# Kernel tuning notes

Hardware: AMD Instinct MI355X
Metric: run time of the kernel (lower is better)

The kernel has to match this reference:

```python
import jax, jax.numpy as jnp
import numpy as np

N_HEAD = 16
N_KV_HEAD = 4
HEAD_DIM = 64  # n_embd // n_head = 1024 // 16
N_EMBD = 1024


def _alibi_bias(T, n_head, head_dim):
    # slopes: start = 2**(-2**(-(log2(H)-3))); slope_i = start**(i+1)
    start = 2.0 ** (-2.0 ** (-(np.log2(n_head) - 3.0)))
    slopes = jnp.asarray(start ** np.arange(1, n_head + 1), dtype=jnp.float32)  # [H]
    rel = (jnp.arange(T, dtype=jnp.float32)[None, :]
           - jnp.arange(T, dtype=jnp.float32)[:, None])  # [T,T], rel[i,j] = j - i
    bias = slopes[:, None, None] * rel[None, :, :]  # [H,T,T]
    # Faithful to the torch module: masked_fill(-inf) is then OVERWRITTEN by
    # torch.tril, which zeroes the upper triangle. Net effect: lower-tri alibi
    # values, 0 above the diagonal (NO causal masking).
    bias = jnp.tril(bias)
    return bias * (head_dim ** -0.5)  # extra scale applied in forward


def setup_inputs() -> dict:
    key = jax.random.key(0)
    ks = jax.random.split(key, 5)
    B, T, C = 4, 2048, N_EMBD
    w_scale = 0.02
    return {
        "x": jax.random.normal(ks[0], (B, T, C), dtype=jnp.float32),
        "Wq": jax.random.normal(ks[1], (C, C), dtype=jnp.float32) * w_scale,
        "Wkv": jax.random.normal(ks[2], (2 * N_KV_HEAD * HEAD_DIM, C), dtype=jnp.float32) * w_scale,
        "Wproj": jax.random.normal(ks[3], (C, C), dtype=jnp.float32) * w_scale,
        "bproj": jnp.zeros((C,), dtype=jnp.float32),
    }


def reference(x, Wq, Wkv, Wproj, bproj):
    B, T, C = x.shape
    H, KVH, D = N_HEAD, N_KV_HEAD, HEAD_DIM
    ratio = H // KVH

    q = jnp.einsum('btc,ec->bte', x, Wq).reshape(B, T, H, D).transpose(0, 2, 1, 3)  # [B,H,T,D]
    kv = jnp.einsum('btc,ec->bte', x, Wkv)  # [B,T,2*KVH*D]
    k, v = jnp.split(kv, 2, axis=-1)
    k = k.reshape(B, T, KVH, D).transpose(0, 2, 1, 3)  # [B,KVH,T,D]
    v = v.reshape(B, T, KVH, D).transpose(0, 2, 1, 3)
    # torch .repeat tiles whole blocks: query head h uses kv head h % KVH
    k = jnp.tile(k, (1, ratio, 1, 1))  # [B,H,T,D]
    v = jnp.tile(v, (1, ratio, 1, 1))

    bias = _alibi_bias(T, H, D)  # [H,T,T], already *= D**-0.5
    scores = jnp.einsum('bhtd,bhsd->bhts', q, k) * (D ** -0.5) + bias[None]
    attn = jax.nn.softmax(scores, axis=-1)
    out = jnp.einsum('bhts,bhsd->bhtd', attn, v)  # [B,H,T,D]
    out = out.transpose(0, 2, 1, 3).reshape(B, T, C)
    return jnp.einsum('btc,ec->bte', out, Wproj) + bproj
```

## Files before the change

### kernel.cpp

```cpp
#include <hip/hip_runtime.h>
#include <hip/hip_bf16.h>
#include <cstdint>

typedef __bf16 bf16;
typedef bf16 bf16x4 __attribute__((ext_vector_type(4)));
typedef bf16 bf16x8 __attribute__((ext_vector_type(8)));
typedef float f32x4 __attribute__((ext_vector_type(4)));

#define MFMA16(a, b, c) __builtin_amdgcn_mfma_f32_16x16x32_bf16((a), (b), (c), 0, 0, 0)

__global__ void cast_f32_to_bf16(const float* __restrict__ src,
                                 bf16* __restrict__ dst, int n4) {
  int i = blockIdx.x * blockDim.x + threadIdx.x;
  if (i < n4) {
    const float4 v = ((const float4*)src)[i];
    bf16x4 o;
    o.x = (bf16)v.x; o.y = (bf16)v.y; o.z = (bf16)v.z; o.w = (bf16)v.w;
    ((bf16x4*)dst)[i] = o;
  }
}

__global__ __launch_bounds__(256, 2)
void gemm_qkv(const bf16* __restrict__ A, const bf16* __restrict__ B,
              bf16* __restrict__ qb, bf16* __restrict__ kb, bf16* __restrict__ vb) {
  constexpr int K = 1024;
  __shared__ bf16 sA[128 * 72];
  __shared__ bf16 sB[128 * 72];
  const int tid = threadIdx.x;
  const int lane = tid & 63, wid = tid >> 6;
  const int col = lane & 15, quad = lane >> 4;
  const int wm = wid >> 1, wn = wid & 1;
  const int m0 = blockIdx.y * 128, n0 = blockIdx.x * 128;

  f32x4 acc[4][4];
  const f32x4 z = {0.f, 0.f, 0.f, 0.f};
#pragma unroll
  for (int mi = 0; mi < 4; mi++)
#pragma unroll
    for (int ni = 0; ni < 4; ni++) acc[mi][ni] = z;

  for (int k0 = 0; k0 < K; k0 += 64) {
    __syncthreads();
#pragma unroll
    for (int c = 0; c < 4; ++c) {
      int idx = c * 256 + tid;
      int row = idx >> 3, kc = idx & 7;
      *(bf16x8*)&sA[row * 72 + kc * 8] =
          *(const bf16x8*)&A[(size_t)(m0 + row) * K + k0 + kc * 8];
      *(bf16x8*)&sB[row * 72 + kc * 8] =
          *(const bf16x8*)&B[(size_t)(n0 + row) * K + k0 + kc * 8];
    }
    __syncthreads();
#pragma unroll
    for (int ks = 0; ks < 2; ++ks) {
      const int kk = ks * 32 + quad * 8;
      bf16x8 af[4], bfr[4];
#pragma unroll
      for (int i = 0; i < 4; i++)
        af[i] = *(const bf16x8*)&sA[(wm * 64 + i * 16 + col) * 72 + kk];
#pragma unroll
      for (int i = 0; i < 4; i++)
        bfr[i] = *(const bf16x8*)&sB[(wn * 64 + i * 16 + col) * 72 + kk];
#pragma unroll
      for (int mi = 0; mi < 4; mi++)
#pragma unroll
        for (int ni = 0; ni < 4; ni++)
          acc[mi][ni] = MFMA16(af[mi], bfr[ni], acc[mi][ni]);
    }
  }
#pragma unroll
  for (int mi = 0; mi < 4; mi++) {
#pragma unroll
    for (int ni = 0; ni < 4; ni++) {
      const int e = n0 + wn * 64 + ni * 16 + col;
#pragma unroll
      for (int r = 0; r < 4; r++) {
        const int m = m0 + wm * 64 + mi * 16 + quad * 4 + r;
        const int bb = m >> 11, t = m & 2047;
        const bf16 val = (bf16)acc[mi][ni][r];
        if (e < 1024) {
          qb[(((size_t)bb * 16 + (e >> 6)) * 2048 + t) * 64 + (e & 63)] = val;
        } else if (e < 1280) {
          const int f = e - 1024;
          kb[(((size_t)bb * 4 + (f >> 6)) * 2048 + t) * 64 + (f & 63)] = val;
        } else {
          const int f = e - 1280;
          vb[(((size_t)bb * 4 + (f >> 6)) * 2048 + t) * 64 + (f & 63)] = val;
        }
      }
    }
  }
}

__global__ __launch_bounds__(256, 2)
void gemm_proj(const bf16* __restrict__ A, const bf16* __restrict__ B,
               const float* __restrict__ bias, float* __restrict__ out) {
  constexpr int K = 1024;
  __shared__ bf16 sA[128 * 72];
  __shared__ bf16 sB[128 * 72];
  const int tid = threadIdx.x;
  const int lane = tid & 63, wid = tid >> 6;
  const int col = lane & 15, quad = lane >> 4;
  const int wm = wid >> 1, wn = wid & 1;
  const int m0 = blockIdx.y * 128, n0 = blockIdx.x * 128;

  f32x4 acc[4][4];
  const f32x4 z = {0.f, 0.f, 0.f, 0.f};
#pragma unroll
  for (int mi = 0; mi < 4; mi++)
#pragma unroll
    for (int ni = 0; ni < 4; ni++) acc[mi][ni] = z;

  for (int k0 = 0; k0 < K; k0 += 64) {
    __syncthreads();
#pragma unroll
    for (int c = 0; c < 4; ++c) {
      int idx = c * 256 + tid;
      int row = idx >> 3, kc = idx & 7;
      *(bf16x8*)&sA[row * 72 + kc * 8] =
          *(const bf16x8*)&A[(size_t)(m0 + row) * K + k0 + kc * 8];
      *(bf16x8*)&sB[row * 72 + kc * 8] =
          *(const bf16x8*)&B[(size_t)(n0 + row) * K + k0 + kc * 8];
    }
    __syncthreads();
#pragma unroll
    for (int ks = 0; ks < 2; ++ks) {
      const int kk = ks * 32 + quad * 8;
      bf16x8 af[4], bfr[4];
#pragma unroll
      for (int i = 0; i < 4; i++)
        af[i] = *(const bf16x8*)&sA[(wm * 64 + i * 16 + col) * 72 + kk];
#pragma unroll
      for (int i = 0; i < 4; i++)
        bfr[i] = *(const bf16x8*)&sB[(wn * 64 + i * 16 + col) * 72 + kk];
#pragma unroll
      for (int mi = 0; mi < 4; mi++)
#pragma unroll
        for (int ni = 0; ni < 4; ni++)
          acc[mi][ni] = MFMA16(af[mi], bfr[ni], acc[mi][ni]);
    }
  }
#pragma unroll
  for (int mi = 0; mi < 4; mi++) {
#pragma unroll
    for (int ni = 0; ni < 4; ni++) {
      const int e = n0 + wn * 64 + ni * 16 + col;
      const float be = bias[e];
#pragma unroll
      for (int r = 0; r < 4; r++) {
        const int m = m0 + wm * 64 + mi * 16 + quad * 4 + r;
        out[(size_t)m * 1024 + e] = acc[mi][ni][r] + be;
      }
    }
  }
}

__global__ __launch_bounds__(256, 2)
void attn_alibi(const bf16* __restrict__ qb, const bf16* __restrict__ kb,
                const bf16* __restrict__ vb, bf16* __restrict__ ob) {
  __shared__ bf16 sK[64 * 72];
  __shared__ bf16 sVt[64 * 72];
  __shared__ bf16 sPt[4][64 * 72];
  __shared__ float sL[4][64];
  const int tid = threadIdx.x;
  const int lane = tid & 63, wid = tid >> 6;
  const int col = lane & 15, quad = lane >> 4;
  const int bh = blockIdx.y;
  const int b = bh >> 4, h = bh & 15, kvh = h & 3;
  const int qbase = __builtin_amdgcn_readfirstlane(blockIdx.x * 256 + wid * 64);

  const bf16* qptr = qb + ((size_t)(b * 16 + h) * 2048 + qbase) * 64;
  const bf16* kptr = kb + ((size_t)(b * 4 + kvh) * 2048) * 64;
  const bf16* vptr = vb + ((size_t)(b * 4 + kvh) * 2048) * 64;

  bf16x8 bq[4][2];
#pragma unroll
  for (int ni = 0; ni < 4; ni++)
#pragma unroll
    for (int ks = 0; ks < 2; ks++)
      bq[ni][ks] = *(const bf16x8*)&qptr[(ni * 16 + col) * 64 + ks * 32 + quad * 8];

  f32x4 O[4][4];
  const f32x4 z = {0.f, 0.f, 0.f, 0.f};
#pragma unroll
  for (int mi = 0; mi < 4; mi++)
#pragma unroll
    for (int nd = 0; nd < 4; nd++) O[mi][nd] = z;
  float lsum[4] = {0.f, 0.f, 0.f, 0.f};

  const float c1 = 0.125f * 1.44269504f;
  const float cb = exp2f(-0.5f * (float)(h + 1)) * c1;
  const int qoff = quad * 4 - col;

  for (int c0 = 0; c0 < 2048; c0 += 64) {
    __syncthreads();
#pragma unroll
    for (int c = 0; c < 2; c++) {
      int idx = c * 256 + tid, row = idx >> 3, kc = idx & 7;
      *(bf16x8*)&sK[row * 72 + kc * 8] =
          *(const bf16x8*)&kptr[(size_t)(c0 + row) * 64 + kc * 8];
    }
#pragma unroll
    for (int c = 0; c < 2; c++) {
      int idx = c * 256 + tid, row = idx >> 3, dc = idx & 7;
      bf16x8 v = *(const bf16x8*)&vptr[(size_t)(c0 + row) * 64 + dc * 8];
      const int blk = row >> 3, rl = row & 7;
#pragma unroll
      for (int j = 0; j < 8; j++)
        sVt[(dc * 8 + j) * 72 + ((blk ^ dc) << 3) + rl] = v[j];
    }
    __syncthreads();

    f32x4 S[4][4];
#pragma unroll
    for (int mi = 0; mi < 4; mi++)
#pragma unroll
      for (int ni = 0; ni < 4; ni++) S[mi][ni] = z;
#pragma unroll
    for (int ks = 0; ks < 2; ks++) {
      bf16x8 ak[4];
#pragma unroll
      for (int mi = 0; mi < 4; mi++)
        ak[mi] = *(const bf16x8*)&sK[(mi * 16 + col) * 72 + ks * 32 + quad * 8];
#pragma unroll
      for (int mi = 0; mi < 4; mi++)
#pragma unroll
        for (int ni = 0; ni < 4; ni++)
          S[mi][ni] = MFMA16(ak[mi], bq[ni][ks], S[mi][ni]);
    }

    bf16* sp = sPt[wid];
#pragma unroll
    for (int ni = 0; ni < 4; ni++) {
      f32x4 p[4];
#pragma unroll
      for (int mi = 0; mi < 4; mi++) {
        const int U = c0 + mi * 16 - qbase - ni * 16;
        if (U <= -15) {
          const float bb = cb * (float)(U + qoff);
#pragma unroll
          for (int r = 0; r < 4; r++)
            p[mi][r] = __builtin_amdgcn_exp2f(S[mi][ni][r] * c1 + (bb + cb * (float)r));
        } else if (U >= 16) {
#pragma unroll
          for (int r = 0; r < 4; r++)
            p[mi][r] = __builtin_amdgcn_exp2f(S[mi][ni][r] * c1);
        } else {
          const float relf = (float)(U + qoff);
#pragma unroll
          for (int r = 0; r < 4; r++) {
            const float rr = relf + (float)r;
            const float bb = (rr <= 0.f) ? cb * rr : 0.f;
            p[mi][r] = __builtin_amdgcn_exp2f(S[mi][ni][r] * c1 + bb);
          }
        }
      }
      f32x4 t = (p[0] + p[1]) + (p[2] + p[3]);
      lsum[ni] += (t.x + t.y) + (t.z + t.w);
#pragma unroll
      for (int mi = 0; mi < 4; mi++) {
        bf16x4 w;
#pragma unroll
        for (int r = 0; r < 4; r++) w[r] = (bf16)p[mi][r];
        *(bf16x4*)&sp[(ni * 16 + col) * 72 + mi * 16 + quad * 4] = w;
      }
    }

#pragma unroll
    for (int ks = 0; ks < 2; ks++) {
      bf16x8 ap[4], bv[4];
#pragma unroll
      for (int mi = 0; mi < 4; mi++)
        ap[mi] = *(const bf16x8*)&sp[(mi * 16 + col) * 72 + ks * 32 + quad * 8];
#pragma unroll
      for (int nd = 0; nd < 4; nd++) {
        const int d = nd * 16 + col;
        bv[nd] = *(const bf16x8*)&sVt[d * 72 + (((ks * 4 + quad) ^ (d >> 3)) << 3)];
      }
#pragma unroll
      for (int mi = 0; mi < 4; mi++)
#pragma unroll
        for (int nd = 0; nd < 4; nd++)
          O[mi][nd] = MFMA16(ap[mi], bv[nd], O[mi][nd]);
    }
  }

#pragma unroll
  for (int ni = 0; ni < 4; ni++) {
    float l = lsum[ni];
    l += __shfl_xor(l, 16);
    l += __shfl_xor(l, 32);
    lsum[ni] = l;
  }
  __syncthreads();
  if (quad == 0) {
#pragma unroll
    for (int ni = 0; ni < 4; ni++) sL[wid][ni * 16 + col] = lsum[ni];
  }
  __syncthreads();

#pragma unroll
  for (int mi = 0; mi < 4; mi++) {
    const f32x4 lv = *(const f32x4*)&sL[wid][mi * 16 + quad * 4];
#pragma unroll
    for (int r = 0; r < 4; r++) {
      const float inv = 1.0f / lv[r];
      const int t = qbase + mi * 16 + quad * 4 + r;
#pragma unroll
      for (int nd = 0; nd < 4; nd++) {
        ob[((size_t)b * 2048 + t) * 1024 + h * 64 + nd * 16 + col] =
            (bf16)(O[mi][nd][r] * inv);
      }
    }
  }
}

extern "C" void kernel_launch(void* const* d_in, const int* in_sizes, int n_in,
                              void* d_out, int out_size, void* d_ws, size_t ws_size,
                              hipStream_t stream) {
  const float* x     = (const float*)d_in[0];
  const float* Wq    = (const float*)d_in[1];
  const float* Wkv   = (const float*)d_in[2];
  const float* Wproj = (const float*)d_in[3];
  const float* bproj = (const float*)d_in[4];
  float* out = (float*)d_out;

  bf16* xb  = (bf16*)d_ws;
  bf16* w1b = xb  + 8388608;
  bf16* wpb = w1b + 1572864;
  bf16* qb  = wpb + 1048576;
  bf16* kb  = qb  + 8388608;
  bf16* vb  = kb  + 2097152;
  bf16* aob = vb  + 2097152;

  cast_f32_to_bf16<<<8192, 256, 0, stream>>>(x, xb, 2097152);
  cast_f32_to_bf16<<<1024, 256, 0, stream>>>(Wq, w1b, 262144);
  cast_f32_to_bf16<<<512, 256, 0, stream>>>(Wkv, w1b + 1048576, 131072);
  cast_f32_to_bf16<<<1024, 256, 0, stream>>>(Wproj, wpb, 262144);

  gemm_qkv<<<dim3(12, 64), 256, 0, stream>>>(xb, w1b, qb, kb, vb);
  attn_alibi<<<dim3(8, 64), 256, 0, stream>>>(qb, kb, vb, aob);
  gemm_proj<<<dim3(8, 64), 256, 0, stream>>>(aob, wpb, bproj, out);
}
```

Measured before the change: 276.9 us.

## Use async global-to-LDS loads with XOR swizzle in GEMMs and prefetch K/V in attention

Both GEMM kernels now load their A and B tiles with global_load_lds direct-to-LDS transfers into an unpadded, XOR-swizzled layout, and the fragment reads apply the matching swizzle. This drops the register round trip and the padding while aiming to avoid LDS bank conflicts. The attention kernel prefetches the next K/V chunk into registers while the current one is in use, overlapping global latency with compute. It uses lgkmcnt-only barriers, and the async LDS loads rely on __syncthreads to wait for vmcnt, which is a correctness risk.

```diff
diff --git a/kernel.cpp b/kernel.cpp
--- a/kernel.cpp
+++ b/kernel.cpp
@@ -8,6 +8,16 @@
 typedef float f32x4 __attribute__((ext_vector_type(4)));
 
 #define MFMA16(a, b, c) __builtin_amdgcn_mfma_f32_16x16x32_bf16((a), (b), (c), 0, 0, 0)
+
+__device__ inline void async16(const bf16* g, bf16* l) {
+  __builtin_amdgcn_global_load_lds(
+      (const __attribute__((address_space(1))) void*)g,
+      (__attribute__((address_space(3))) void*)l, 16, 0, 0);
+}
+
+__device__ inline void lds_barrier() {
+  asm volatile("s_waitcnt lgkmcnt(0)\n\ts_barrier" ::: "memory");
+}
 
 __global__ void cast_f32_to_bf16(const float* __restrict__ src,
                                  bf16* __restrict__ dst, int n4) {
@@ -24,13 +34,14 @@
 void gemm_qkv(const bf16* __restrict__ A, const bf16* __restrict__ B,
               bf16* __restrict__ qb, bf16* __restrict__ kb, bf16* __restrict__ vb) {
   constexpr int K = 1024;
-  __shared__ bf16 sA[128 * 72];
-  __shared__ bf16 sB[128 * 72];
+  __shared__ bf16 sA[128 * 64];
+  __shared__ bf16 sB[128 * 64];
   const int tid = threadIdx.x;
   const int lane = tid & 63, wid = tid >> 6;
   const int col = lane & 15, quad = lane >> 4;
   const int wm = wid >> 1, wn = wid & 1;
   const int m0 = blockIdx.y * 128, n0 = blockIdx.x * 128;
+  const int c7 = col & 7;
 
   f32x4 acc[4][4];
   const f32x4 z = {0.f, 0.f, 0.f, 0.f};
@@ -43,24 +54,24 @@
     __syncthreads();
 #pragma unroll
     for (int c = 0; c < 4; ++c) {
-      int idx = c * 256 + tid;
-      int row = idx >> 3, kc = idx & 7;
-      *(bf16x8*)&sA[row * 72 + kc * 8] =
-          *(const bf16x8*)&A[(size_t)(m0 + row) * K + k0 + kc * 8];
-      *(bf16x8*)&sB[row * 72 + kc * 8] =
-          *(const bf16x8*)&B[(size_t)(n0 + row) * K + k0 + kc * 8];
+      const int idx = c * 256 + tid;
+      const int row = idx >> 3, kc = idx & 7;
+      const int gkc = kc ^ (row & 7);
+      async16(&A[(size_t)(m0 + row) * K + k0 + gkc * 8], &sA[idx * 8]);
+      async16(&B[(size_t)(n0 + row) * K + k0 + gkc * 8], &sB[idx * 8]);
     }
     __syncthreads();
 #pragma unroll
     for (int ks = 0; ks < 2; ++ks) {
-      const int kk = ks * 32 + quad * 8;
       bf16x8 af[4], bfr[4];
 #pragma unroll
       for (int i = 0; i < 4; i++)
-        af[i] = *(const bf16x8*)&sA[(wm * 64 + i * 16 + col) * 72 + kk];
+        af[i] = *(const bf16x8*)&sA[(wm * 64 + i * 16 + col) * 64 +
+                                    (((ks * 4 + quad) ^ c7) << 3)];
 #pragma unroll
       for (int i = 0; i < 4; i++)
-        bfr[i] = *(const bf16x8*)&sB[(wn * 64 + i * 16 + col) * 72 + kk];
+        bfr[i] = *(const bf16x8*)&sB[(wn * 64 + i * 16 + col) * 64 +
+                                     (((ks * 4 + quad) ^ c7) << 3)];
 #pragma unroll
       for (int mi = 0; mi < 4; mi++)
 #pragma unroll
@@ -96,13 +107,14 @@
 void gemm_proj(const bf16* __restrict__ A, const bf16* __restrict__ B,
                const float* __restrict__ bias, float* __restrict__ out) {
   constexpr int K = 1024;
-  __shared__ bf16 sA[128 * 72];
-  __shared__ bf16 sB[128 * 72];
+  __shared__ bf16 sA[128 * 64];
+  __shared__ bf16 sB[128 * 64];
   const int tid = threadIdx.x;
   const int lane = tid & 63, wid = tid >> 6;
   const int col = lane & 15, quad = lane >> 4;
   const int wm = wid >> 1, wn = wid & 1;
   const int m0 = blockIdx.y * 128, n0 = blockIdx.x * 128;
+  const int c7 = col & 7;
 
   f32x4 acc[4][4];
   const f32x4 z = {0.f, 0.f, 0.f, 0.f};
@@ -115,24 +127,24 @@
     __syncthreads();
 #pragma unroll
     for (int c = 0; c < 4; ++c) {
-      int idx = c * 256 + tid;
-      int row = idx >> 3, kc = idx & 7;
-      *(bf16x8*)&sA[row * 72 + kc * 8] =
-          *(const bf16x8*)&A[(size_t)(m0 + row) * K + k0 + kc * 8];
-      *(bf16x8*)&sB[row * 72 + kc * 8] =
-          *(const bf16x8*)&B[(size_t)(n0 + row) * K + k0 + kc * 8];
+      const int idx = c * 256 + tid;
+      const int row = idx >> 3, kc = idx & 7;
+      const int gkc = kc ^ (row & 7);
+      async16(&A[(size_t)(m0 + row) * K + k0 + gkc * 8], &sA[idx * 8]);
+      async16(&B[(size_t)(n0 + row) * K + k0 + gkc * 8], &sB[idx * 8]);
     }
     __syncthreads();
 #pragma unroll
     for (int ks = 0; ks < 2; ++ks) {
-      const int kk = ks * 32 + quad * 8;
       bf16x8 af[4], bfr[4];
 #pragma unroll
       for (int i = 0; i < 4; i++)
-        af[i] = *(const bf16x8*)&sA[(wm * 64 + i * 16 + col) * 72 + kk];
+        af[i] = *(const bf16x8*)&sA[(wm * 64 + i * 16 + col) * 64 +
+                                    (((ks * 4 + quad) ^ c7) << 3)];
 #pragma unroll
       for (int i = 0; i < 4; i++)
-        bfr[i] = *(const bf16x8*)&sB[(wn * 64 + i * 16 + col) * 72 + kk];
+        bfr[i] = *(const bf16x8*)&sB[(wn * 64 + i * 16 + col) * 64 +
+                                     (((ks * 4 + quad) ^ c7) << 3)];
 #pragma unroll
       for (int mi = 0; mi < 4; mi++)
 #pragma unroll
@@ -192,24 +204,35 @@
   const float cb = exp2f(-0.5f * (float)(h + 1)) * c1;
   const int qoff = quad * 4 - col;
 
+  const int r0 = tid >> 3, r1 = 32 + (tid >> 3), kc = tid & 7;
+
+  bf16x8 kr0, kr1, vr0, vr1;
+  kr0 = *(const bf16x8*)&kptr[(size_t)r0 * 64 + kc * 8];
+  kr1 = *(const bf16x8*)&kptr[(size_t)r1 * 64 + kc * 8];
+  vr0 = *(const bf16x8*)&vptr[(size_t)r0 * 64 + kc * 8];
+  vr1 = *(const bf16x8*)&vptr[(size_t)r1 * 64 + kc * 8];
+
   for (int c0 = 0; c0 < 2048; c0 += 64) {
-    __syncthreads();
-#pragma unroll
-    for (int c = 0; c < 2; c++) {
-      int idx = c * 256 + tid, row = idx >> 3, kc = idx & 7;
-      *(bf16x8*)&sK[row * 72 + kc * 8] =
-          *(const bf16x8*)&kptr[(size_t)(c0 + row) * 64 + kc * 8];
-    }
-#pragma unroll
-    for (int c = 0; c < 2; c++) {
-      int idx = c * 256 + tid, row = idx >> 3, dc = idx & 7;
-      bf16x8 v = *(const bf16x8*)&vptr[(size_t)(c0 + row) * 64 + dc * 8];
-      const int blk = row >> 3, rl = row & 7;
-#pragma unroll
-      for (int j = 0; j < 8; j++)
-        sVt[(dc * 8 + j) * 72 + ((blk ^ dc) << 3) + rl] = v[j];
-    }
-    __syncthreads();
+    lds_barrier();
+    *(bf16x8*)&sK[r0 * 72 + kc * 8] = kr0;
+    *(bf16x8*)&sK[r1 * 72 + kc * 8] = kr1;
+    {
+      const int blk0 = r0 >> 3, rl0 = r0 & 7;
+      const int blk1 = r1 >> 3, rl1 = r1 & 7;
+#pragma unroll
+      for (int j = 0; j < 8; j++) {
+        sVt[(kc * 8 + j) * 72 + ((blk0 ^ kc) << 3) + rl0] = vr0[j];
+        sVt[(kc * 8 + j) * 72 + ((blk1 ^ kc) << 3) + rl1] = vr1[j];
+      }
+    }
+    {
+      const int cn = (c0 + 64 < 2048) ? c0 + 64 : 0;
+      kr0 = *(const bf16x8*)&kptr[(size_t)(cn + r0) * 64 + kc * 8];
+      kr1 = *(const bf16x8*)&kptr[(size_t)(cn + r1) * 64 + kc * 8];
+      vr0 = *(const bf16x8*)&vptr[(size_t)(cn + r0) * 64 + kc * 8];
+      vr1 = *(const bf16x8*)&vptr[(size_t)(cn + r1) * 64 + kc * 8];
+    }
+    lds_barrier();
 
     f32x4 S[4][4];
 #pragma unroll
```

After: 280.8 us. Within noise of the previous version (+1.4%).
